# Kernel optimization log

Measured on AMD Instinct MI355X. Metric: run time of the kernel, lower is better.

The kernel has to match this reference:

```python
import jax, jax.numpy as jnp
import numpy as np

D_MODEL = 2048
N_HEADS = 16
N_KV_HEADS = 4
HEAD_DIM = D_MODEL // N_HEADS  # 128
WINDOW = 512
THETA = 10000.0


def rotate_half(x):
    x1, x2 = jnp.split(x, 2, axis=-1)
    return jnp.concatenate((-x2, x1), axis=-1)


def rope_cos_sin(seq_len, dtype=jnp.float32):
    inv_freq = 1.0 / (THETA ** (jnp.arange(0, HEAD_DIM, 2, dtype=jnp.float32) / HEAD_DIM))
    t = jnp.arange(seq_len, dtype=jnp.float32)
    freqs = jnp.outer(t, inv_freq)              # [S, HEAD_DIM/2]
    emb = jnp.concatenate((freqs, freqs), -1)   # [S, HEAD_DIM]
    return jnp.cos(emb).astype(dtype), jnp.sin(emb).astype(dtype)


def setup_inputs() -> dict:
    key = jax.random.key(0)
    ks = jax.random.split(key, 5)
    B, S = 2, 2048
    sc = 1.0 / np.sqrt(D_MODEL)
    return {
        "x": jax.random.normal(ks[0], (B, S, D_MODEL), jnp.float32),
        "wq": jax.random.normal(ks[1], (D_MODEL, N_HEADS * HEAD_DIM), jnp.float32) * sc,
        "wk": jax.random.normal(ks[2], (D_MODEL, N_KV_HEADS * HEAD_DIM), jnp.float32) * sc,
        "wv": jax.random.normal(ks[3], (D_MODEL, N_KV_HEADS * HEAD_DIM), jnp.float32) * sc,
        "wo": jax.random.normal(ks[4], (N_HEADS * HEAD_DIM, D_MODEL), jnp.float32) * sc,
    }


def reference(x, wq, wk, wv, wo):
    B, S, _ = x.shape
    n_rep = N_HEADS // N_KV_HEADS

    q = (x @ wq).reshape(B, S, N_HEADS, HEAD_DIM).transpose(0, 2, 1, 3)      # [B,H,S,D]
    k = (x @ wk).reshape(B, S, N_KV_HEADS, HEAD_DIM).transpose(0, 2, 1, 3)   # [B,KVH,S,D]
    v = (x @ wv).reshape(B, S, N_KV_HEADS, HEAD_DIM).transpose(0, 2, 1, 3)

    cos, sin = rope_cos_sin(S, x.dtype)  # [S, D]
    q = q * cos + rotate_half(q) * sin
    k = k * cos + rotate_half(k) * sin

    # GQA: repeat kv heads to match query heads
    k = jnp.repeat(k, n_rep, axis=1)  # [B,H,S,D]
    v = jnp.repeat(v, n_rep, axis=1)

    scale = 1.0 / np.sqrt(HEAD_DIM)
    scores = jnp.einsum("bhqd,bhkd->bhqk", q, k) * scale

    # causal + sliding-window mask: allow i-WINDOW+1 <= j <= i
    i = jnp.arange(S)[:, None]
    j = jnp.arange(S)[None, :]
    allowed = (j <= i) & (j >= i - WINDOW + 1)
    scores = jnp.where(allowed, scores, -jnp.inf)

    attn = jax.nn.softmax(scores.astype(jnp.float32), axis=-1).astype(x.dtype)
    out = jnp.einsum("bhqk,bhkd->bhqd", attn, v)          # [B,H,S,D]
    out = out.transpose(0, 2, 1, 3).reshape(B, S, N_HEADS * HEAD_DIM)
    return out @ wo
```

## Files before the change

kernel.cpp:

```cpp
#include <hip/hip_runtime.h>
#include <math.h>


typedef unsigned short u16;
typedef __attribute__((ext_vector_type(4))) float f32x4;
typedef __attribute__((ext_vector_type(8))) __bf16 bf16x8;
typedef __attribute__((ext_vector_type(4))) __bf16 bf16x4;
typedef __attribute__((ext_vector_type(4))) short s16x4;
typedef __attribute__((ext_vector_type(8))) unsigned short u16x8;
typedef __attribute__((ext_vector_type(4))) unsigned short u16x4;

#define DEV static __device__ __forceinline__

DEV float bf2f(u16 h) {
    union { unsigned int i; float f; } x;
    x.i = ((unsigned int)h) << 16;
    return x.f;
}
DEV u16 f2bf(float f) {
    union { float f; unsigned int i; } x;
    x.f = f;
    unsigned int u = x.i;
    return (u16)((u + 0x7FFFu + ((u >> 16) & 1u)) >> 16);
}

DEV f32x4 mfma32(bf16x8 a, bf16x8 b, f32x4 c) {
    return __builtin_amdgcn_mfma_f32_16x16x32_bf16(a, b, c, 0, 0, 0);
}
DEV f32x4 mfma16(bf16x4 a, bf16x4 b, f32x4 c) {
#if __has_builtin(__builtin_amdgcn_mfma_f32_16x16x16_bf16)
    return __builtin_amdgcn_mfma_f32_16x16x16_bf16(a, b, c, 0, 0, 0);
#else
    union { bf16x4 v; s16x4 s; } ua, ub;
    ua.v = a; ub.v = b;
    return __builtin_amdgcn_mfma_f32_16x16x16bf16_1k(ua.s, ub.s, c, 0, 0, 0);
#endif
}

DEV void gload_lds16(const void* g, void* lds) {
    __builtin_amdgcn_global_load_lds(
        (const __attribute__((address_space(1))) unsigned int*)g,
        (__attribute__((address_space(3))) unsigned int*)lds, 16, 0, 0);
}

__global__ __launch_bounds__(256) void sincos_kernel(float* ct, float* st) {
    int idx = blockIdx.x * 256 + threadIdx.x;
    int s = idx >> 6, d = idx & 63;
    float inv = exp2f(-(float)d * (13.287712379549449f / 64.f));
    float a = (float)s * inv;
    float sv, cv;
    sincosf(a, &sv, &cv);
    ct[idx] = cv;
    st[idx] = sv;
}

__global__ __launch_bounds__(256) void f32_to_bf16_kernel(const float* in, u16* out, int n4) {
    int i = blockIdx.x * 256 + threadIdx.x;
    if (i >= n4) return;
    float4 v = ((const float4*)in)[i];
    u16x4 o;
    o[0] = f2bf(v.x); o[1] = f2bf(v.y); o[2] = f2bf(v.z); o[3] = f2bf(v.w);
    ((u16x4*)out)[i] = o;
}

__global__ __launch_bounds__(256) void convT_kernel(const float* in, int ldi, u16* out, int ldo) {
    __shared__ float tile[32][33];
    int cc = threadIdx.x & 31, rb = threadIdx.x >> 5;
    long r0 = (long)blockIdx.y * 32, c0 = (long)blockIdx.x * 32;
#pragma unroll
    for (int i = 0; i < 4; i++)
        tile[rb + i * 8][cc] = in[(r0 + rb + i * 8) * (long)ldi + c0 + cc];
    __syncthreads();
#pragma unroll
    for (int i = 0; i < 4; i++)
        out[(c0 + rb + i * 8) * (long)ldo + r0 + cc] = f2bf(tile[cc][rb + i * 8]);
}

__global__ __launch_bounds__(256) void transpose_bf16_kernel(const u16* in, int ldi, long in_bs,
                                                             u16* out, int ldo, long out_bs) {
    __shared__ u16 tile[32][33];
    in += (long)blockIdx.z * in_bs;
    out += (long)blockIdx.z * out_bs;
    int cc = threadIdx.x & 31, rb = threadIdx.x >> 5;
    long r0 = (long)blockIdx.y * 32, c0 = (long)blockIdx.x * 32;
#pragma unroll
    for (int i = 0; i < 4; i++)
        tile[rb + i * 8][cc] = in[(r0 + rb + i * 8) * (long)ldi + c0 + cc];
    __syncthreads();
#pragma unroll
    for (int i = 0; i < 4; i++)
        out[(c0 + rb + i * 8) * (long)ldo + r0 + cc] = tile[cc][rb + i * 8];
}

__global__ __launch_bounds__(256) void rope_kernel(u16* base, int ld, int nheads,
                                                   const float* ct, const float* st, int total) {
    int idx = blockIdx.x * 256 + threadIdx.x;
    if (idx >= total) return;
    int per_row = nheads * 8;
    int m = idx / per_row;
    int rest = idx - m * per_row;
    int hh = rest >> 3;
    int d0 = (rest & 7) * 8;
    int s = m & 2047;
    u16* p1 = base + (long)m * ld + hh * 128 + d0;
    u16* p2 = p1 + 64;
    u16x8 v1 = *(const u16x8*)p1;
    u16x8 v2 = *(const u16x8*)p2;
    const float* cp = ct + s * 64 + d0;
    const float* sp = st + s * 64 + d0;
    u16x8 o1, o2;
#pragma unroll
    for (int j = 0; j < 8; j++) {
        float x1 = bf2f(v1[j]), x2 = bf2f(v2[j]);
        float cc = cp[j], ss = sp[j];
        o1[j] = f2bf(x1 * cc - x2 * ss);
        o2[j] = f2bf(x2 * cc + x1 * ss);
    }
    *(u16x8*)p1 = o1;
    *(u16x8*)p2 = o2;
}

template <bool OUT_BF16>
__global__ __launch_bounds__(256) void gemm_bt_kernel(const u16* A, const u16* Bt, void* Cout,
                                                      int M, int N, int K) {
    __shared__ u16 As[2][128 * 32];
    __shared__ u16 Bs[2][128 * 32];
    const int tid = threadIdx.x;
    const int w = tid >> 6, l = tid & 63, g = l >> 4, c = l & 15;
    const int wm = w >> 1, wn = w & 1;
    const long m0 = (long)blockIdx.y * 128, n0 = (long)blockIdx.x * 128;
    const int nk = K >> 5;

    f32x4 acc[4][4];
    const f32x4 zero = {0.f, 0.f, 0.f, 0.f};
#pragma unroll
    for (int i = 0; i < 4; i++)
#pragma unroll
        for (int j = 0; j < 4; j++) acc[i][j] = zero;

    auto stage = [&](int buf, int kt) {
#pragma unroll
        for (int i = 0; i < 2; i++) {
            int o = (i * 256 + tid) * 16;
            int row = o >> 6;
            int cl = ((o >> 4) & 3) ^ ((row >> 1) & 3);
            gload_lds16(A + (m0 + row) * (long)K + kt * 32 + cl * 8,
                        (void*)&As[buf][(i * 256 + w * 64) * 8]);
        }
#pragma unroll
        for (int i = 0; i < 2; i++) {
            int o = (i * 256 + tid) * 16;
            int row = o >> 6;
            int cl = ((o >> 4) & 3) ^ ((row >> 1) & 3);
            gload_lds16(Bt + (n0 + row) * (long)K + kt * 32 + cl * 8,
                        (void*)&Bs[buf][(i * 256 + w * 64) * 8]);
        }
    };

    stage(0, 0);
    __syncthreads();
    int buf = 0;
    for (int kt = 0; kt < nk; ++kt) {
        if (kt + 1 < nk) stage(buf ^ 1, kt + 1);
        bf16x8 af[4], bf[4];
#pragma unroll
        for (int i = 0; i < 4; i++) {
            int rowa = wm * 64 + i * 16 + c;
            int cha = g ^ ((rowa >> 1) & 3);
            af[i] = *(const bf16x8*)&As[buf][rowa * 32 + cha * 8];
            int rowb = wn * 64 + i * 16 + c;
            int chb = g ^ ((rowb >> 1) & 3);
            bf[i] = *(const bf16x8*)&Bs[buf][rowb * 32 + chb * 8];
        }
#pragma unroll
        for (int i = 0; i < 4; i++)
#pragma unroll
            for (int j = 0; j < 4; j++) acc[i][j] = mfma32(af[i], bf[j], acc[i][j]);
        __syncthreads();
        buf ^= 1;
    }

#pragma unroll
    for (int i = 0; i < 4; i++)
#pragma unroll
        for (int j = 0; j < 4; j++) {
            long row0 = m0 + wm * 64 + i * 16 + g * 4;
            long col = n0 + wn * 64 + j * 16 + c;
#pragma unroll
            for (int r = 0; r < 4; r++) {
                float v = acc[i][j][r];
                if (OUT_BF16)
                    ((u16*)Cout)[(row0 + r) * (long)N + col] = f2bf(v);
                else
                    ((float*)Cout)[(row0 + r) * (long)N + col] = v;
            }
        }
}

#define ATT_SCALE 0.08838834764831845f
#define L2E 1.4426950408889634f

__global__ __launch_bounds__(256) void attn_kernel(const u16* QKV, const u16* Vt, u16* AO) {
    __shared__ u16 Ks[64 * 128];
    __shared__ u16 Vs[128 * 64];
    const int tid = threadIdx.x;
    const int w = tid >> 6, l = tid & 63, g = l >> 4, c = l & 15;
    const int Tq = blockIdx.x;
    const int h = blockIdx.y;
    const int b = blockIdx.z;
    const int kvh = h >> 2;
    const int q0 = Tq * 64;
    const int qb = q0 + w * 16;

    bf16x8 bq[4];
    {
        const u16* qrow = QKV + (long)(b * 2048 + qb + c) * 3072 + h * 128;
#pragma unroll
        for (int kc = 0; kc < 4; kc++) bq[kc] = *(const bf16x8*)(qrow + kc * 32 + g * 8);
    }

    f32x4 acc_o[8];
    const f32x4 zero = {0.f, 0.f, 0.f, 0.f};
#pragma unroll
    for (int i = 0; i < 8; i++) acc_o[i] = zero;
    float m_run = -3.0e38f, l_run = 0.f;

    const int t_lo = (q0 > 511) ? ((q0 - 511) >> 6) : 0;
    const int t_hi = Tq;

    for (int t = t_lo; t <= t_hi; ++t) {
        const int kv0 = t * 64;
#pragma unroll
        for (int i = 0; i < 4; i++) {
            int o = (i * 256 + tid) * 16;
            int key = o >> 8;
            int cl = ((o >> 4) & 15) ^ (key & 15);
            gload_lds16(QKV + (long)(b * 2048 + kv0 + key) * 3072 + 2048 + kvh * 128 + cl * 8,
                        (void*)&Ks[(i * 256 + w * 64) * 8]);
        }
#pragma unroll
        for (int i = 0; i < 4; i++) {
            int o = (i * 256 + tid) * 16;
            int d = o >> 7;
            int cl = ((o >> 4) & 7) ^ (d & 7);
            gload_lds16(Vt + (long)((b * 4 + kvh) * 128 + d) * 2048 + kv0 + cl * 8,
                        (void*)&Vs[(i * 256 + w * 64) * 8]);
        }
        __syncthreads();

        f32x4 sacc[4];
#pragma unroll
        for (int n = 0; n < 4; n++) {
            sacc[n] = zero;
#pragma unroll
            for (int kc = 0; kc < 4; kc++) {
                int row = n * 16 + c;
                int ch = (kc * 4 + g) ^ c;
                bf16x8 kf = *(const bf16x8*)&Ks[row * 128 + ch * 8];
                sacc[n] = mfma32(kf, bq[kc], sacc[n]);
            }
        }

        const bool edge = (kv0 + 63 > qb) || (kv0 < qb + 15 - 511);
        float p[4][4];
        float m_tile = -3.0e38f;
#pragma unroll
        for (int n = 0; n < 4; n++)
#pragma unroll
            for (int r = 0; r < 4; r++) {
                float s = sacc[n][r] * ATT_SCALE;
                if (edge) {
                    int j = kv0 + n * 16 + 4 * g + r;
                    int q = qb + c;
                    if (j > q || j < q - 511) s = -__builtin_inff();
                }
                p[n][r] = s;
                m_tile = fmaxf(m_tile, s);
            }
        m_tile = fmaxf(m_tile, __shfl_xor(m_tile, 16));
        m_tile = fmaxf(m_tile, __shfl_xor(m_tile, 32));
        float m_new = fmaxf(m_run, m_tile);
        float alpha = exp2f((m_run - m_new) * L2E);
        float lsum = 0.f;
#pragma unroll
        for (int n = 0; n < 4; n++)
#pragma unroll
            for (int r = 0; r < 4; r++) {
                float e = exp2f((p[n][r] - m_new) * L2E);
                p[n][r] = e;
                lsum += e;
            }
        lsum += __shfl_xor(lsum, 16);
        lsum += __shfl_xor(lsum, 32);
        l_run = l_run * alpha + lsum;
        m_run = m_new;

        float alpha_r[4];
#pragma unroll
        for (int r = 0; r < 4; r++) alpha_r[r] = __shfl(alpha, (g << 4) + 4 * g + r);
#pragma unroll
        for (int dn = 0; dn < 8; dn++) {
            f32x4 t2 = acc_o[dn];
            t2[0] *= alpha_r[0]; t2[1] *= alpha_r[1];
            t2[2] *= alpha_r[2]; t2[3] *= alpha_r[3];
            acc_o[dn] = t2;
        }

        bf16x4 ap[4];
#pragma unroll
        for (int n = 0; n < 4; n++) {
            union { u16x4 u; bf16x4 b; } pk;
            pk.u[0] = f2bf(p[n][0]); pk.u[1] = f2bf(p[n][1]);
            pk.u[2] = f2bf(p[n][2]); pk.u[3] = f2bf(p[n][3]);
            ap[n] = pk.b;
        }

#pragma unroll
        for (int n = 0; n < 4; n++)
#pragma unroll
            for (int dn = 0; dn < 8; dn++) {
                int row = dn * 16 + c;
                int ch = (2 * n + (g >> 1)) ^ (c & 7);
                bf16x4 vf = *(const bf16x4*)&Vs[row * 64 + ch * 8 + (g & 1) * 4];
                acc_o[dn] = mfma16(ap[n], vf, acc_o[dn]);
            }
        __syncthreads();
    }

    float lr[4];
#pragma unroll
    for (int r = 0; r < 4; r++) {
        float lq = __shfl(l_run, (g << 4) + 4 * g + r);
        lr[r] = 1.f / lq;
    }
#pragma unroll
    for (int dn = 0; dn < 8; dn++)
#pragma unroll
        for (int r = 0; r < 4; r++) {
            long row = (long)(b * 2048 + qb + 4 * g + r);
            AO[row * 2048 + h * 128 + dn * 16 + c] = f2bf(acc_o[dn][r] * lr[r]);
        }
}

extern "C" void kernel_launch(void* const* d_in, const int* in_sizes, int n_in,
                              void* d_out, int out_size, void* d_ws, size_t ws_size,
                              hipStream_t stream) {
    const float* x = (const float*)d_in[0];
    const float* wq = (const float*)d_in[1];
    const float* wk = (const float*)d_in[2];
    const float* wv = (const float*)d_in[3];
    const float* wo = (const float*)d_in[4];
    float* out = (float*)d_out;

    char* ws = (char*)d_ws;
    u16* xb = (u16*)(ws);
    u16* wAll = (u16*)(ws + 16777216);
    u16* woT = (u16*)(ws + 29360128);
    u16* QKV = (u16*)(ws + 37748736);
    u16* Vt = (u16*)(ws + 62914560);
    u16* AO = (u16*)(ws + 67108864);
    float* ct = (float*)(ws + 83886080);
    float* st = (float*)(ws + 84410368);

    sincos_kernel<<<512, 256, 0, stream>>>(ct, st);
    f32_to_bf16_kernel<<<8192, 256, 0, stream>>>(x, xb, 2097152);
    convT_kernel<<<dim3(64, 64), 256, 0, stream>>>(wq, 2048, wAll, 2048);
    convT_kernel<<<dim3(16, 64), 256, 0, stream>>>(wk, 512, wAll + (long)2048 * 2048, 2048);
    convT_kernel<<<dim3(16, 64), 256, 0, stream>>>(wv, 512, wAll + (long)2560 * 2048, 2048);
    convT_kernel<<<dim3(64, 64), 256, 0, stream>>>(wo, 2048, woT, 2048);

    gemm_bt_kernel<true><<<dim3(24, 32), 256, 0, stream>>>(xb, wAll, QKV, 4096, 3072, 2048);

    rope_kernel<<<2048, 256, 0, stream>>>(QKV, 3072, 16, ct, st, 524288);
    rope_kernel<<<512, 256, 0, stream>>>(QKV + 2048, 3072, 4, ct, st, 131072);

    transpose_bf16_kernel<<<dim3(16, 64, 2), 256, 0, stream>>>(
        QKV + 2560, 3072, (long)2048 * 3072, Vt, 2048, (long)512 * 2048);

    attn_kernel<<<dim3(32, 16, 2), 256, 0, stream>>>(QKV, Vt, AO);

    gemm_bt_kernel<false><<<dim3(16, 32), 256, 0, stream>>>(AO, woT, out, 4096, 2048, 2048);
}
```

Measured before the change: 205.5 us.

## Replace GEMMs with 4-stage pipelined 256-row tiles, fuse V transpose and launches

Replaces the double-buffered 128x128 GEMM with a 512-thread, 256-row-tile kernel that keeps a 4-deep LDS ring, using explicit vmcnt waits, raw barriers and raised wave priority around the MFMA block. The QKV GEMM epilogue now writes V straight into the transposed Vt layout, so the separate transpose kernel goes away. The four weight convert-transposes are merged into one launch and the two RoPE launches into one. This trades more LDS and registers per block, and hard-coded shape constants, for fewer launches and better latency hiding in the GEMMs.

```diff
diff --git a/kernel.cpp b/kernel.cpp
--- a/kernel.cpp
+++ b/kernel.cpp
@@ -11,6 +11,7 @@
 typedef __attribute__((ext_vector_type(4))) unsigned short u16x4;
 
 #define DEV static __device__ __forceinline__
+#define WAITV(n) asm volatile("s_waitcnt vmcnt(" #n ")" ::: "memory")
 
 DEV float bf2f(u16 h) {
     union { unsigned int i; float f; } x;
@@ -63,8 +64,15 @@
     ((u16x4*)out)[i] = o;
 }
 
-__global__ __launch_bounds__(256) void convT_kernel(const float* in, int ldi, u16* out, int ldo) {
+__global__ __launch_bounds__(256) void convT4_kernel(const float* i0, const float* i1,
+                                                     const float* i2, const float* i3,
+                                                     u16* o0, u16* o1, u16* o2, u16* o3) {
     __shared__ float tile[32][33];
+    int z = blockIdx.z;
+    const float* in = (z == 0) ? i0 : (z == 1) ? i1 : (z == 2) ? i2 : i3;
+    u16* out = (z == 0) ? o0 : (z == 1) ? o1 : (z == 2) ? o2 : o3;
+    int ldi = (z == 1 || z == 2) ? 512 : 2048;
+    if ((int)blockIdx.x >= (ldi >> 5)) return;
     int cc = threadIdx.x & 31, rb = threadIdx.x >> 5;
     long r0 = (long)blockIdx.y * 32, c0 = (long)blockIdx.x * 32;
 #pragma unroll
@@ -73,36 +81,26 @@
     __syncthreads();
 #pragma unroll
     for (int i = 0; i < 4; i++)
-        out[(c0 + rb + i * 8) * (long)ldo + r0 + cc] = f2bf(tile[cc][rb + i * 8]);
-}
-
-__global__ __launch_bounds__(256) void transpose_bf16_kernel(const u16* in, int ldi, long in_bs,
-                                                             u16* out, int ldo, long out_bs) {
-    __shared__ u16 tile[32][33];
-    in += (long)blockIdx.z * in_bs;
-    out += (long)blockIdx.z * out_bs;
-    int cc = threadIdx.x & 31, rb = threadIdx.x >> 5;
-    long r0 = (long)blockIdx.y * 32, c0 = (long)blockIdx.x * 32;
-#pragma unroll
-    for (int i = 0; i < 4; i++)
-        tile[rb + i * 8][cc] = in[(r0 + rb + i * 8) * (long)ldi + c0 + cc];
-    __syncthreads();
-#pragma unroll
-    for (int i = 0; i < 4; i++)
-        out[(c0 + rb + i * 8) * (long)ldo + r0 + cc] = tile[cc][rb + i * 8];
-}
-
-__global__ __launch_bounds__(256) void rope_kernel(u16* base, int ld, int nheads,
-                                                   const float* ct, const float* st, int total) {
+        out[(c0 + rb + i * 8) * 2048L + r0 + cc] = f2bf(tile[cc][rb + i * 8]);
+}
+
+__global__ __launch_bounds__(256) void rope2_kernel(u16* QKV, const float* ct, const float* st) {
     int idx = blockIdx.x * 256 + threadIdx.x;
-    if (idx >= total) return;
-    int per_row = nheads * 8;
-    int m = idx / per_row;
-    int rest = idx - m * per_row;
-    int hh = rest >> 3;
-    int d0 = (rest & 7) * 8;
+    int m, hoff, d0;
+    if (idx < 524288) {
+        m = idx >> 7;
+        int rest = idx & 127;
+        hoff = (rest >> 3) * 128;
+        d0 = (rest & 7) * 8;
+    } else {
+        int i2 = idx - 524288;
+        m = i2 >> 5;
+        int rest = i2 & 31;
+        hoff = 2048 + (rest >> 3) * 128;
+        d0 = (rest & 7) * 8;
+    }
     int s = m & 2047;
-    u16* p1 = base + (long)m * ld + hh * 128 + d0;
+    u16* p1 = QKV + (long)m * 3072 + hoff + d0;
     u16* p2 = p1 + 64;
     u16x8 v1 = *(const u16x8*)p1;
     u16x8 v2 = *(const u16x8*)p2;
@@ -120,81 +118,136 @@
     *(u16x8*)p2 = o2;
 }
 
-template <bool OUT_BF16>
-__global__ __launch_bounds__(256) void gemm_bt_kernel(const u16* A, const u16* Bt, void* Cout,
-                                                      int M, int N, int K) {
-    __shared__ u16 As[2][128 * 32];
-    __shared__ u16 Bs[2][128 * 32];
+template <int BN, int WN, int EPI>
+__global__ __launch_bounds__(512, 2) void gemm_pipe_kernel(const u16* __restrict__ A,
+                                                           const u16* __restrict__ Bt,
+                                                           void* __restrict__ Cout,
+                                                           u16* __restrict__ Vt) {
+    constexpr int WM = 8 / WN;
+    constexpr int M_REP = (256 / WM) / 16;
+    constexpr int N_REP = (BN / WN) / 16;
+    constexpr int SC_B = (BN * 64) / 8192;
+    constexpr int SC = 2 + SC_B;
+    constexpr int BUFSZ = 8192 + BN * 32;
+    constexpr int NK = 64;
+
+    __shared__ u16 lds[4 * BUFSZ];
     const int tid = threadIdx.x;
     const int w = tid >> 6, l = tid & 63, g = l >> 4, c = l & 15;
-    const int wm = w >> 1, wn = w & 1;
-    const long m0 = (long)blockIdx.y * 128, n0 = (long)blockIdx.x * 128;
-    const int nk = K >> 5;
-
-    f32x4 acc[4][4];
+    const int wr = w / WN, wc = w % WN;
+    const long m0 = (long)blockIdx.y * 256, n0 = (long)blockIdx.x * BN;
+
+    const u16* srcA[2];
+    const u16* srcB[SC_B];
+#pragma unroll
+    for (int j = 0; j < 2; j++) {
+        int x = j * 8192 + tid * 16;
+        int row = ((x >> 10) << 4) | ((x >> 4) & 15);
+        int g8 = ((x >> 8) & 3) * 8;
+        srcA[j] = A + (size_t)(m0 + row) * 2048 + g8;
+    }
+#pragma unroll
+    for (int j = 0; j < SC_B; j++) {
+        int x = j * 8192 + tid * 16;
+        int row = ((x >> 10) << 4) | ((x >> 4) & 15);
+        int g8 = ((x >> 8) & 3) * 8;
+        srcB[j] = Bt + (size_t)(n0 + row) * 2048 + g8;
+    }
+
+    auto stage = [&](int t) {
+        const int bb = t & 3;
+#pragma unroll
+        for (int j = 0; j < 2; j++)
+            gload_lds16(srcA[j] + t * 32, (void*)&lds[bb * BUFSZ + j * 4096 + tid * 8]);
+#pragma unroll
+        for (int j = 0; j < SC_B; j++)
+            gload_lds16(srcB[j] + t * 32, (void*)&lds[bb * BUFSZ + 8192 + j * 4096 + tid * 8]);
+    };
+
+    f32x4 acc[M_REP][N_REP];
     const f32x4 zero = {0.f, 0.f, 0.f, 0.f};
 #pragma unroll
-    for (int i = 0; i < 4; i++)
-#pragma unroll
-        for (int j = 0; j < 4; j++) acc[i][j] = zero;
-
-    auto stage = [&](int buf, int kt) {
-#pragma unroll
-        for (int i = 0; i < 2; i++) {
-            int o = (i * 256 + tid) * 16;
-            int row = o >> 6;
-            int cl = ((o >> 4) & 3) ^ ((row >> 1) & 3);
-            gload_lds16(A + (m0 + row) * (long)K + kt * 32 + cl * 8,
-                        (void*)&As[buf][(i * 256 + w * 64) * 8]);
-        }
-#pragma unroll
-        for (int i = 0; i < 2; i++) {
-            int o = (i * 256 + tid) * 16;
-            int row = o >> 6;
-            int cl = ((o >> 4) & 3) ^ ((row >> 1) & 3);
-            gload_lds16(Bt + (n0 + row) * (long)K + kt * 32 + cl * 8,
-                        (void*)&Bs[buf][(i * 256 + w * 64) * 8]);
-        }
-    };
-
-    stage(0, 0);
-    __syncthreads();
-    int buf = 0;
-    for (int kt = 0; kt < nk; ++kt) {
-        if (kt + 1 < nk) stage(buf ^ 1, kt + 1);
-        bf16x8 af[4], bf[4];
-#pragma unroll
-        for (int i = 0; i < 4; i++) {
-            int rowa = wm * 64 + i * 16 + c;
-            int cha = g ^ ((rowa >> 1) & 3);
-            af[i] = *(const bf16x8*)&As[buf][rowa * 32 + cha * 8];
-            int rowb = wn * 64 + i * 16 + c;
-            int chb = g ^ ((rowb >> 1) & 3);
-            bf[i] = *(const bf16x8*)&Bs[buf][rowb * 32 + chb * 8];
-        }
-#pragma unroll
-        for (int i = 0; i < 4; i++)
-#pragma unroll
-            for (int j = 0; j < 4; j++) acc[i][j] = mfma32(af[i], bf[j], acc[i][j]);
-        __syncthreads();
-        buf ^= 1;
-    }
-
-#pragma unroll
-    for (int i = 0; i < 4; i++)
-#pragma unroll
-        for (int j = 0; j < 4; j++) {
-            long row0 = m0 + wm * 64 + i * 16 + g * 4;
-            long col = n0 + wn * 64 + j * 16 + c;
-#pragma unroll
-            for (int r = 0; r < 4; r++) {
-                float v = acc[i][j][r];
-                if (OUT_BF16)
-                    ((u16*)Cout)[(row0 + r) * (long)N + col] = f2bf(v);
-                else
-                    ((float*)Cout)[(row0 + r) * (long)N + col] = v;
+    for (int i = 0; i < M_REP; i++)
+#pragma unroll
+        for (int j = 0; j < N_REP; j++) acc[i][j] = zero;
+
+    stage(0);
+    stage(1);
+    stage(2);
+
+    for (int kt = 0; kt < NK; ++kt) {
+        const int buf = kt & 3;
+        if (kt <= NK - 3) {
+            if constexpr (SC == 4) WAITV(8); else WAITV(6);
+        } else if (kt == NK - 2) {
+            if constexpr (SC == 4) WAITV(4); else WAITV(3);
+        } else {
+            WAITV(0);
+        }
+        __builtin_amdgcn_s_barrier();
+        __builtin_amdgcn_sched_barrier(0);
+        asm volatile("" ::: "memory");
+
+        if (kt + 3 < NK) stage(kt + 3);
+
+        const u16* bp = &lds[buf * BUFSZ];
+        bf16x8 af[M_REP], bfr[N_REP];
+#pragma unroll
+        for (int nj = 0; nj < N_REP; nj++)
+            bfr[nj] = *(const bf16x8*)&bp[8192 + (wc * N_REP + nj) * 512 + l * 8];
+#pragma unroll
+        for (int mi = 0; mi < M_REP; mi++)
+            af[mi] = *(const bf16x8*)&bp[(wr * M_REP + mi) * 512 + l * 8];
+
+        __builtin_amdgcn_s_setprio(1);
+#pragma unroll
+        for (int mi = 0; mi < M_REP; mi++)
+#pragma unroll
+            for (int nj = 0; nj < N_REP; nj++)
+                acc[mi][nj] = mfma32(af[mi], bfr[nj], acc[mi][nj]);
+        __builtin_amdgcn_s_setprio(0);
+    }
+
+    if (EPI == 0) {
+        float* C = (float*)Cout;
+#pragma unroll
+        for (int mi = 0; mi < M_REP; mi++)
+#pragma unroll
+            for (int nj = 0; nj < N_REP; nj++) {
+                long row0 = m0 + wr * (256 / WM) + mi * 16 + g * 4;
+                long col = n0 + wc * (BN / WN) + nj * 16 + c;
+#pragma unroll
+                for (int r = 0; r < 4; r++)
+                    C[(row0 + r) * 2048 + col] = acc[mi][nj][r];
             }
-        }
+    } else {
+        u16* Cq = (u16*)Cout;
+        if (n0 < 2560) {
+#pragma unroll
+            for (int mi = 0; mi < M_REP; mi++)
+#pragma unroll
+                for (int nj = 0; nj < N_REP; nj++) {
+                    long row0 = m0 + wr * (256 / WM) + mi * 16 + g * 4;
+                    long col = n0 + wc * (BN / WN) + nj * 16 + c;
+#pragma unroll
+                    for (int r = 0; r < 4; r++)
+                        Cq[(row0 + r) * 3072 + col] = f2bf(acc[mi][nj][r]);
+                }
+        } else {
+#pragma unroll
+            for (int mi = 0; mi < M_REP; mi++)
+#pragma unroll
+                for (int nj = 0; nj < N_REP; nj++) {
+                    long row0 = m0 + wr * (256 / WM) + mi * 16 + g * 4;
+                    long b = row0 >> 11, s0 = row0 & 2047;
+                    long dglob = n0 + wc * (BN / WN) + nj * 16 + c - 2560;
+                    u16x4 pk;
+                    pk[0] = f2bf(acc[mi][nj][0]); pk[1] = f2bf(acc[mi][nj][1]);
+                    pk[2] = f2bf(acc[mi][nj][2]); pk[3] = f2bf(acc[mi][nj][3]);
+                    *(u16x4*)&Vt[(b * 512 + dglob) * 2048 + s0] = pk;
+                }
+        }
+    }
 }
 
 #define ATT_SCALE 0.08838834764831845f
@@ -364,20 +417,14 @@
 
     sincos_kernel<<<512, 256, 0, stream>>>(ct, st);
     f32_to_bf16_kernel<<<8192, 256, 0, stream>>>(x, xb, 2097152);
-    convT_kernel<<<dim3(64, 64), 256, 0, stream>>>(wq, 2048, wAll, 2048);
-    convT_kernel<<<dim3(16, 64), 256, 0, stream>>>(wk, 512, wAll + (long)2048 * 2048, 2048);
-    convT_kernel<<<dim3(16, 64), 256, 0, stream>>>(wv, 512, wAll + (long)2560 * 2048, 2048);
-    convT_kernel<<<dim3(64, 64), 256, 0, stream>>>(wo, 2048, woT, 2048);
-
-    gemm_bt_kernel<true><<<dim3(24, 32), 256, 0, stream>>>(xb, wAll, QKV, 4096, 3072, 2048);
-
-    rope_kernel<<<2048, 256, 0, stream>>>(QKV, 3072, 16, ct, st, 524288);
-    rope_kernel<<<512, 256, 0, stream>>>(QKV + 2048, 3072, 4, ct, st, 131072);
-
-    transpose_bf16_kernel<<<dim3(16, 64, 2), 256, 0, stream>>>(
-        QKV + 2560, 3072, (long)2048 * 3072, Vt, 2048, (long)512 * 2048);
+    convT4_kernel<<<dim3(64, 64, 4), 256, 0, stream>>>(
+        wq, wk, wv, wo, wAll, wAll + (long)2048 * 2048, wAll + (long)2560 * 2048, woT);
+
+    gemm_pipe_kernel<256, 4, 1><<<dim3(12, 16), 512, 0, stream>>>(xb, wAll, QKV, Vt);
+
+    rope2_kernel<<<2560, 256, 0, stream>>>(QKV, ct, st);
 
     attn_kernel<<<dim3(32, 16, 2), 256, 0, stream>>>(QKV, Vt, AO);
 
-    gemm_bt_kernel<false><<<dim3(16, 32), 256, 0, stream>>>(AO, woT, out, 4096, 2048, 2048);
-}
+    gemm_pipe_kernel<128, 2, 0><<<dim3(16, 16), 512, 0, stream>>>(AO, woT, out, nullptr);
+}
```

Result: no change. 208.9 us (+1.7%).

## Merge prep kernels, fuse V transpose into QKV GEMM, double-buffer attention

Applied to the files above, without the earlier changes.

Six preprocessing launches (sincos, x conversion, four weight transposes) become one prep kernel, and the two RoPE launches become one. The QKV GEMM epilogue writes V straight into transposed layout, which removes the separate transpose kernel. The attention kernel now uses 512 threads covering 128 queries and double-buffers K/V tiles in LDS, prefetching the next tile while computing the current one. Tiles a warp does not need are skipped per warp. The cost is fewer, larger attention blocks, more LDS per block and scattered 8-byte V stores.

```diff
diff --git a/kernel.cpp b/kernel.cpp
--- a/kernel.cpp
+++ b/kernel.cpp
@@ -43,66 +43,68 @@
         (__attribute__((address_space(3))) unsigned int*)lds, 16, 0, 0);
 }
 
-__global__ __launch_bounds__(256) void sincos_kernel(float* ct, float* st) {
-    int idx = blockIdx.x * 256 + threadIdx.x;
-    int s = idx >> 6, d = idx & 63;
-    float inv = exp2f(-(float)d * (13.287712379549449f / 64.f));
-    float a = (float)s * inv;
-    float sv, cv;
-    sincosf(a, &sv, &cv);
-    ct[idx] = cv;
-    st[idx] = sv;
-}
-
-__global__ __launch_bounds__(256) void f32_to_bf16_kernel(const float* in, u16* out, int n4) {
-    int i = blockIdx.x * 256 + threadIdx.x;
-    if (i >= n4) return;
-    float4 v = ((const float4*)in)[i];
-    u16x4 o;
-    o[0] = f2bf(v.x); o[1] = f2bf(v.y); o[2] = f2bf(v.z); o[3] = f2bf(v.w);
-    ((u16x4*)out)[i] = o;
-}
-
-__global__ __launch_bounds__(256) void convT_kernel(const float* in, int ldi, u16* out, int ldo) {
+__global__ __launch_bounds__(256) void prep_kernel(const float* x, const float* wq,
+                                                   const float* wk, const float* wv,
+                                                   const float* wo, u16* xb, u16* wAll,
+                                                   u16* woT, float* ct, float* st) {
     __shared__ float tile[32][33];
-    int cc = threadIdx.x & 31, rb = threadIdx.x >> 5;
-    long r0 = (long)blockIdx.y * 32, c0 = (long)blockIdx.x * 32;
+    const int bid = blockIdx.x;
+    const int tid = threadIdx.x;
+    if (bid < 512) {
+        int idx = bid * 256 + tid;
+        int s = idx >> 6, d = idx & 63;
+        float inv = exp2f(-(float)d * (13.287712379549449f / 64.f));
+        float a = (float)s * inv;
+        float sv, cv;
+        sincosf(a, &sv, &cv);
+        ct[idx] = cv;
+        st[idx] = sv;
+        return;
+    }
+    if (bid < 8704) {
+        int i = (bid - 512) * 256 + tid;
+        float4 v = ((const float4*)x)[i];
+        u16x4 o;
+        o[0] = f2bf(v.x); o[1] = f2bf(v.y); o[2] = f2bf(v.z); o[3] = f2bf(v.w);
+        ((u16x4*)xb)[i] = o;
+        return;
+    }
+    int r = bid - 8704;
+    const float* in;
+    u16* out;
+    int ldi, bx, by;
+    if (r < 4096) { in = wq; out = wAll; ldi = 2048; bx = r & 63; by = r >> 6; }
+    else if (r < 5120) { r -= 4096; in = wk; out = wAll + (long)2048 * 2048; ldi = 512; bx = r & 15; by = r >> 4; }
+    else if (r < 6144) { r -= 5120; in = wv; out = wAll + (long)2560 * 2048; ldi = 512; bx = r & 15; by = r >> 4; }
+    else { r -= 6144; in = wo; out = woT; ldi = 2048; bx = r & 63; by = r >> 6; }
+    int cc = tid & 31, rb = tid >> 5;
+    long r0 = (long)by * 32, c0 = (long)bx * 32;
 #pragma unroll
     for (int i = 0; i < 4; i++)
         tile[rb + i * 8][cc] = in[(r0 + rb + i * 8) * (long)ldi + c0 + cc];
     __syncthreads();
 #pragma unroll
     for (int i = 0; i < 4; i++)
-        out[(c0 + rb + i * 8) * (long)ldo + r0 + cc] = f2bf(tile[cc][rb + i * 8]);
-}
-
-__global__ __launch_bounds__(256) void transpose_bf16_kernel(const u16* in, int ldi, long in_bs,
-                                                             u16* out, int ldo, long out_bs) {
-    __shared__ u16 tile[32][33];
-    in += (long)blockIdx.z * in_bs;
-    out += (long)blockIdx.z * out_bs;
-    int cc = threadIdx.x & 31, rb = threadIdx.x >> 5;
-    long r0 = (long)blockIdx.y * 32, c0 = (long)blockIdx.x * 32;
-#pragma unroll
-    for (int i = 0; i < 4; i++)
-        tile[rb + i * 8][cc] = in[(r0 + rb + i * 8) * (long)ldi + c0 + cc];
-    __syncthreads();
-#pragma unroll
-    for (int i = 0; i < 4; i++)
-        out[(c0 + rb + i * 8) * (long)ldo + r0 + cc] = tile[cc][rb + i * 8];
-}
-
-__global__ __launch_bounds__(256) void rope_kernel(u16* base, int ld, int nheads,
-                                                   const float* ct, const float* st, int total) {
+        out[(c0 + rb + i * 8) * 2048L + r0 + cc] = f2bf(tile[cc][rb + i * 8]);
+}
+
+__global__ __launch_bounds__(256) void rope2_kernel(u16* QKV, const float* ct, const float* st) {
     int idx = blockIdx.x * 256 + threadIdx.x;
-    if (idx >= total) return;
-    int per_row = nheads * 8;
-    int m = idx / per_row;
-    int rest = idx - m * per_row;
-    int hh = rest >> 3;
-    int d0 = (rest & 7) * 8;
+    int m, hoff, d0;
+    if (idx < 524288) {
+        m = idx >> 7;
+        int rest = idx & 127;
+        hoff = (rest >> 3) * 128;
+        d0 = (rest & 7) * 8;
+    } else {
+        int i2 = idx - 524288;
+        m = i2 >> 5;
+        int rest = i2 & 31;
+        hoff = 2048 + (rest >> 3) * 128;
+        d0 = (rest & 7) * 8;
+    }
     int s = m & 2047;
-    u16* p1 = base + (long)m * ld + hh * 128 + d0;
+    u16* p1 = QKV + (long)m * 3072 + hoff + d0;
     u16* p2 = p1 + 64;
     u16x8 v1 = *(const u16x8*)p1;
     u16x8 v2 = *(const u16x8*)p2;
@@ -120,9 +122,9 @@
     *(u16x8*)p2 = o2;
 }
 
-template <bool OUT_BF16>
+template <int EPI>
 __global__ __launch_bounds__(256) void gemm_bt_kernel(const u16* A, const u16* Bt, void* Cout,
-                                                      int M, int N, int K) {
+                                                      u16* Vt, int M, int N, int K) {
     __shared__ u16 As[2][128 * 32];
     __shared__ u16 Bs[2][128 * 32];
     const int tid = threadIdx.x;
@@ -180,36 +182,60 @@
         buf ^= 1;
     }
 
-#pragma unroll
-    for (int i = 0; i < 4; i++)
-#pragma unroll
-        for (int j = 0; j < 4; j++) {
-            long row0 = m0 + wm * 64 + i * 16 + g * 4;
-            long col = n0 + wn * 64 + j * 16 + c;
-#pragma unroll
-            for (int r = 0; r < 4; r++) {
-                float v = acc[i][j][r];
-                if (OUT_BF16)
-                    ((u16*)Cout)[(row0 + r) * (long)N + col] = f2bf(v);
-                else
-                    ((float*)Cout)[(row0 + r) * (long)N + col] = v;
+    if (EPI == 0) {
+        float* C = (float*)Cout;
+#pragma unroll
+        for (int i = 0; i < 4; i++)
+#pragma unroll
+            for (int j = 0; j < 4; j++) {
+                long row0 = m0 + wm * 64 + i * 16 + g * 4;
+                long col = n0 + wn * 64 + j * 16 + c;
+#pragma unroll
+                for (int r = 0; r < 4; r++)
+                    C[(row0 + r) * (long)N + col] = acc[i][j][r];
             }
-        }
+    } else {
+        u16* Cq = (u16*)Cout;
+        if (n0 < 2560) {
+#pragma unroll
+            for (int i = 0; i < 4; i++)
+#pragma unroll
+                for (int j = 0; j < 4; j++) {
+                    long row0 = m0 + wm * 64 + i * 16 + g * 4;
+                    long col = n0 + wn * 64 + j * 16 + c;
+#pragma unroll
+                    for (int r = 0; r < 4; r++)
+                        Cq[(row0 + r) * 3072 + col] = f2bf(acc[i][j][r]);
+                }
+        } else {
+#pragma unroll
+            for (int i = 0; i < 4; i++)
+#pragma unroll
+                for (int j = 0; j < 4; j++) {
+                    long row0 = m0 + wm * 64 + i * 16 + g * 4;
+                    long bb = row0 >> 11, s0 = row0 & 2047;
+                    long dglob = n0 + wn * 64 + j * 16 + c - 2560;
+                    u16x4 pk;
+                    pk[0] = f2bf(acc[i][j][0]); pk[1] = f2bf(acc[i][j][1]);
+                    pk[2] = f2bf(acc[i][j][2]); pk[3] = f2bf(acc[i][j][3]);
+                    *(u16x4*)&Vt[(bb * 512 + dglob) * 2048 + s0] = pk;
+                }
+        }
+    }
 }
 
 #define ATT_SCALE 0.08838834764831845f
 #define L2E 1.4426950408889634f
 
-__global__ __launch_bounds__(256) void attn_kernel(const u16* QKV, const u16* Vt, u16* AO) {
-    __shared__ u16 Ks[64 * 128];
-    __shared__ u16 Vs[128 * 64];
+__global__ __launch_bounds__(512) void attn_kernel(const u16* QKV, const u16* Vt, u16* AO) {
+    __shared__ u16 Ks[2][64 * 128];
+    __shared__ u16 Vs[2][128 * 64];
     const int tid = threadIdx.x;
     const int w = tid >> 6, l = tid & 63, g = l >> 4, c = l & 15;
-    const int Tq = blockIdx.x;
     const int h = blockIdx.y;
     const int b = blockIdx.z;
     const int kvh = h >> 2;
-    const int q0 = Tq * 64;
+    const int q0 = blockIdx.x * 128;
     const int qb = q0 + w * 16;
 
     bf16x8 bq[4];
@@ -226,105 +252,117 @@
     float m_run = -3.0e38f, l_run = 0.f;
 
     const int t_lo = (q0 > 511) ? ((q0 - 511) >> 6) : 0;
-    const int t_hi = Tq;
-
-    for (int t = t_lo; t <= t_hi; ++t) {
+    const int t_hi = (q0 + 127) >> 6;
+
+    auto stage = [&](int sb, int t) {
         const int kv0 = t * 64;
 #pragma unroll
-        for (int i = 0; i < 4; i++) {
-            int o = (i * 256 + tid) * 16;
+        for (int i = 0; i < 2; i++) {
+            int o = (i * 512 + tid) * 16;
             int key = o >> 8;
             int cl = ((o >> 4) & 15) ^ (key & 15);
             gload_lds16(QKV + (long)(b * 2048 + kv0 + key) * 3072 + 2048 + kvh * 128 + cl * 8,
-                        (void*)&Ks[(i * 256 + w * 64) * 8]);
-        }
-#pragma unroll
-        for (int i = 0; i < 4; i++) {
-            int o = (i * 256 + tid) * 16;
+                        (void*)&Ks[sb][(i * 512 + w * 64) * 8]);
+        }
+#pragma unroll
+        for (int i = 0; i < 2; i++) {
+            int o = (i * 512 + tid) * 16;
             int d = o >> 7;
             int cl = ((o >> 4) & 7) ^ (d & 7);
             gload_lds16(Vt + (long)((b * 4 + kvh) * 128 + d) * 2048 + kv0 + cl * 8,
-                        (void*)&Vs[(i * 256 + w * 64) * 8]);
+                        (void*)&Vs[sb][(i * 512 + w * 64) * 8]);
+        }
+    };
+
+    stage(0, t_lo);
+    __syncthreads();
+    int buf = 0;
+
+    for (int t = t_lo; t <= t_hi; ++t) {
+        const int kv0 = t * 64;
+        if (t < t_hi) stage(buf ^ 1, t + 1);
+
+        const bool active = (kv0 <= qb + 15) && (kv0 + 63 >= qb - 511);
+        if (active) {
+            f32x4 sacc[4];
+#pragma unroll
+            for (int n = 0; n < 4; n++) {
+                sacc[n] = zero;
+#pragma unroll
+                for (int kc = 0; kc < 4; kc++) {
+                    int row = n * 16 + c;
+                    int ch = (kc * 4 + g) ^ c;
+                    bf16x8 kf = *(const bf16x8*)&Ks[buf][row * 128 + ch * 8];
+                    sacc[n] = mfma32(kf, bq[kc], sacc[n]);
+                }
+            }
+
+            const bool edge = (kv0 + 63 > qb) || (kv0 < qb + 15 - 511);
+            float p[4][4];
+            float m_tile = -3.0e38f;
+#pragma unroll
+            for (int n = 0; n < 4; n++)
+#pragma unroll
+                for (int r = 0; r < 4; r++) {
+                    float s = sacc[n][r] * ATT_SCALE;
+                    if (edge) {
+                        int j = kv0 + n * 16 + 4 * g + r;
+                        int q = qb + c;
+                        if (j > q || j < q - 511) s = -__builtin_inff();
+                    }
+                    p[n][r] = s;
+                    m_tile = fmaxf(m_tile, s);
+                }
+            m_tile = fmaxf(m_tile, __shfl_xor(m_tile, 16));
+            m_tile = fmaxf(m_tile, __shfl_xor(m_tile, 32));
+            float m_new = fmaxf(m_run, m_tile);
+            float alpha = exp2f((m_run - m_new) * L2E);
+            float lsum = 0.f;
+#pragma unroll
+            for (int n = 0; n < 4; n++)
+#pragma unroll
+                for (int r = 0; r < 4; r++) {
+                    float e = exp2f((p[n][r] - m_new) * L2E);
+                    p[n][r] = e;
+                    lsum += e;
+                }
+            lsum += __shfl_xor(lsum, 16);
+            lsum += __shfl_xor(lsum, 32);
+            l_run = l_run * alpha + lsum;
+            m_run = m_new;
+
+            float alpha_r[4];
+#pragma unroll
+            for (int r = 0; r < 4; r++) alpha_r[r] = __shfl(alpha, (g << 4) + 4 * g + r);
+#pragma unroll
+            for (int dn = 0; dn < 8; dn++) {
+                f32x4 t2 = acc_o[dn];
+                t2[0] *= alpha_r[0]; t2[1] *= alpha_r[1];
+                t2[2] *= alpha_r[2]; t2[3] *= alpha_r[3];
+                acc_o[dn] = t2;
+            }
+
+            bf16x4 ap[4];
+#pragma unroll
+            for (int n = 0; n < 4; n++) {
+                union { u16x4 u; bf16x4 b; } pk;
+                pk.u[0] = f2bf(p[n][0]); pk.u[1] = f2bf(p[n][1]);
+                pk.u[2] = f2bf(p[n][2]); pk.u[3] = f2bf(p[n][3]);
+                ap[n] = pk.b;
+            }
+
+#pragma unroll
+            for (int n = 0; n < 4; n++)
+#pragma unroll
+                for (int dn = 0; dn < 8; dn++) {
+                    int row = dn * 16 + c;
+                    int ch = (2 * n + (g >> 1)) ^ (c & 7);
+                    bf16x4 vf = *(const bf16x4*)&Vs[buf][row * 64 + ch * 8 + (g & 1) * 4];
+                    acc_o[dn] = mfma16(ap[n], vf, acc_o[dn]);
+                }
         }
         __syncthreads();
-
-        f32x4 sacc[4];
-#pragma unroll
-        for (int n = 0; n < 4; n++) {
-            sacc[n] = zero;
-#pragma unroll
-            for (int kc = 0; kc < 4; kc++) {
-                int row = n * 16 + c;
-                int ch = (kc * 4 + g) ^ c;
-                bf16x8 kf = *(const bf16x8*)&Ks[row * 128 + ch * 8];
-                sacc[n] = mfma32(kf, bq[kc], sacc[n]);
-            }
-        }
-
-        const bool edge = (kv0 + 63 > qb) || (kv0 < qb + 15 - 511);
-        float p[4][4];
-        float m_tile = -3.0e38f;
-#pragma unroll
-        for (int n = 0; n < 4; n++)
-#pragma unroll
-            for (int r = 0; r < 4; r++) {
-                float s = sacc[n][r] * ATT_SCALE;
-                if (edge) {
-                    int j = kv0 + n * 16 + 4 * g + r;
-                    int q = qb + c;
-                    if (j > q || j < q - 511) s = -__builtin_inff();
-                }
-                p[n][r] = s;
-                m_tile = fmaxf(m_tile, s);
-            }
-        m_tile = fmaxf(m_tile, __shfl_xor(m_tile, 16));
-        m_tile = fmaxf(m_tile, __shfl_xor(m_tile, 32));
-        float m_new = fmaxf(m_run, m_tile);
-        float alpha = exp2f((m_run - m_new) * L2E);
-        float lsum = 0.f;
-#pragma unroll
-        for (int n = 0; n < 4; n++)
-#pragma unroll
-            for (int r = 0; r < 4; r++) {
-                float e = exp2f((p[n][r] - m_new) * L2E);
-                p[n][r] = e;
-                lsum += e;
-            }
-        lsum += __shfl_xor(lsum, 16);
-        lsum += __shfl_xor(lsum, 32);
-        l_run = l_run * alpha + lsum;
-        m_run = m_new;
-
-        float alpha_r[4];
-#pragma unroll
-        for (int r = 0; r < 4; r++) alpha_r[r] = __shfl(alpha, (g << 4) + 4 * g + r);
-#pragma unroll
-        for (int dn = 0; dn < 8; dn++) {
-            f32x4 t2 = acc_o[dn];
-            t2[0] *= alpha_r[0]; t2[1] *= alpha_r[1];
-            t2[2] *= alpha_r[2]; t2[3] *= alpha_r[3];
-            acc_o[dn] = t2;
-        }
-
-        bf16x4 ap[4];
-#pragma unroll
-        for (int n = 0; n < 4; n++) {
-            union { u16x4 u; bf16x4 b; } pk;
-            pk.u[0] = f2bf(p[n][0]); pk.u[1] = f2bf(p[n][1]);
-            pk.u[2] = f2bf(p[n][2]); pk.u[3] = f2bf(p[n][3]);
-            ap[n] = pk.b;
-        }
-
-#pragma unroll
-        for (int n = 0; n < 4; n++)
-#pragma unroll
-            for (int dn = 0; dn < 8; dn++) {
-                int row = dn * 16 + c;
-                int ch = (2 * n + (g >> 1)) ^ (c & 7);
-                bf16x4 vf = *(const bf16x4*)&Vs[row * 64 + ch * 8 + (g & 1) * 4];
-                acc_o[dn] = mfma16(ap[n], vf, acc_o[dn]);
-            }
-        __syncthreads();
+        buf ^= 1;
     }
 
     float lr[4];
@@ -362,22 +400,13 @@
     float* ct = (float*)(ws + 83886080);
     float* st = (float*)(ws + 84410368);
 
-    sincos_kernel<<<512, 256, 0, stream>>>(ct, st);
-    f32_to_bf16_kernel<<<8192, 256, 0, stream>>>(x, xb, 2097152);
-    convT_kernel<<<dim3(64, 64), 256, 0, stream>>>(wq, 2048, wAll, 2048);
-    convT_kernel<<<dim3(16, 64), 256, 0, stream>>>(wk, 512, wAll + (long)2048 * 2048, 2048);
-    convT_kernel<<<dim3(16, 64), 256, 0, stream>>>(wv, 512, wAll + (long)2560 * 2048, 2048);
-    convT_kernel<<<dim3(64, 64), 256, 0, stream>>>(wo, 2048, woT, 2048);
-
-    gemm_bt_kernel<true><<<dim3(24, 32), 256, 0, stream>>>(xb, wAll, QKV, 4096, 3072, 2048);
-
-    rope_kernel<<<2048, 256, 0, stream>>>(QKV, 3072, 16, ct, st, 524288);
-    rope_kernel<<<512, 256, 0, stream>>>(QKV + 2048, 3072, 4, ct, st, 131072);
-
-    transpose_bf16_kernel<<<dim3(16, 64, 2), 256, 0, stream>>>(
-        QKV + 2560, 3072, (long)2048 * 3072, Vt, 2048, (long)512 * 2048);
-
-    attn_kernel<<<dim3(32, 16, 2), 256, 0, stream>>>(QKV, Vt, AO);
-
-    gemm_bt_kernel<false><<<dim3(16, 32), 256, 0, stream>>>(AO, woT, out, 4096, 2048, 2048);
-}
+    prep_kernel<<<18944, 256, 0, stream>>>(x, wq, wk, wv, wo, xb, wAll, woT, ct, st);
+
+    gemm_bt_kernel<1><<<dim3(24, 32), 256, 0, stream>>>(xb, wAll, QKV, Vt, 4096, 3072, 2048);
+
+    rope2_kernel<<<2560, 256, 0, stream>>>(QKV, ct, st);
+
+    attn_kernel<<<dim3(16, 16, 2), 512, 0, stream>>>(QKV, Vt, AO);
+
+    gemm_bt_kernel<0><<<dim3(16, 32), 256, 0, stream>>>(AO, woT, out, nullptr, 4096, 2048, 2048);
+}
```

Result: no change. 204.6 us (-0.4%).
